# Optimization experiments

Hardware: AMD Instinct MI355X
Metric: run time of the kernel (lower is better)

Reference implementation:

```python
import jax, jax.numpy as jnp
import numpy as np
import math
from functools import partial

SIGMA0 = 12.0
KSIZE = int(2 * (4.0 * SIGMA0 + 0.5))  # 97, already odd
if KSIZE % 2 == 0:
    KSIZE -= 1


def _gauss1d(ksize, sigma):
    # kornia-style gaussian; ksize is odd so no half-pixel shift
    x = jnp.arange(ksize, dtype=jnp.float32) - ksize // 2
    g = jnp.exp(-(x ** 2) / (2.0 * sigma ** 2))
    return g / g.sum()


def _blur(x, sigma):
    # x: (N,1,H,W). filter2d with outer(kx,ky) kernel and constant(zero) border
    # == two separable 1D convs with zero 'SAME' padding.
    k = _gauss1d(KSIZE, sigma)
    dn = ('NCHW', 'OIHW', 'NCHW')
    x = jax.lax.conv_general_dilated(x, k[None, None, :, None], (1, 1), 'SAME', dimension_numbers=dn)
    x = jax.lax.conv_general_dilated(x, k[None, None, None, :], (1, 1), 'SAME', dimension_numbers=dn)
    return x


def _grid_sample_bilinear(img, grid):
    # img: (N,C,H,W); grid: (N,H,W,2) with last dim (x,y) in [-1,1], align_corners=True
    N, C, H, W = img.shape
    x = (grid[..., 0] + 1.0) * 0.5 * (W - 1)
    y = (grid[..., 1] + 1.0) * 0.5 * (H - 1)
    x0 = jnp.floor(x); y0 = jnp.floor(y)
    wx = x - x0; wy = y - y0
    x0i = jnp.clip(x0, 0, W - 1).astype(jnp.int32)
    x1i = jnp.clip(x0 + 1, 0, W - 1).astype(jnp.int32)
    y0i = jnp.clip(y0, 0, H - 1).astype(jnp.int32)
    y1i = jnp.clip(y0 + 1, 0, H - 1).astype(jnp.int32)
    flat = img.reshape(N, C, H * W)

    def gather(yi, xi):
        idx = (yi * W + xi).reshape(N, 1, H * W)
        return jnp.take_along_axis(flat, idx, axis=2).reshape(N, C, H, W)

    wx = wx[:, None]; wy = wy[:, None]  # broadcast over C
    top = gather(y0i, x0i) * (1 - wx) + gather(y0i, x1i) * wx
    bot = gather(y1i, x0i) * (1 - wx) + gather(y1i, x1i) * wx
    return top * (1 - wy) + bot * wy


def _elastic(t, d_rand, sigma, alpha):
    # t: (1,C,H,W); d_rand: (1,2,H,W) uniform [0,1]
    n, c, h, w = t.shape
    d = d_rand * 2.0 - 1.0
    dy = _blur(d[:, 0:1], sigma[0]) * alpha[0]   # (1,1,H,W)
    dx = _blur(d[:, 1:2], sigma[1]) * alpha[1]
    d_yx = jnp.concatenate([dy, dx], axis=1).transpose(0, 2, 3, 1)  # (1,H,W,2) = (dy,dx)
    xs = jnp.linspace(-1.0, 1.0, w, dtype=t.dtype)
    ys = jnp.linspace(-1.0, 1.0, h, dtype=t.dtype)
    gx, gy = jnp.meshgrid(xs, ys)  # (H,W)
    grid = jnp.stack([gx, gy], axis=-1)[None]  # (1,H,W,2) (x,y)
    # NOTE: faithful to source: dy is added to x-coord, dx to y-coord
    return _grid_sample_bilinear(t, jnp.clip(grid + d_yx, -1.0, 1.0))


def setup_inputs() -> dict:
    key = jax.random.key(0)
    k1, k2, k3 = jax.random.split(key, 3)
    H = W = 2048
    return {
        'image': jax.random.normal(k1, (3, H, W), dtype=jnp.float32),
        'mask': (jax.random.uniform(k2, (1, H, W)) > 0.5).astype(jnp.float32),
        'd_rand': jax.random.uniform(k3, (1, 2, H, W), dtype=jnp.float32),
        'log_sigma': jnp.full((2,), math.log(12.0), dtype=jnp.float32),
        'log_alpha': jnp.zeros((2,), dtype=jnp.float32),
    }


def reference(image, mask, d_rand, log_sigma, log_alpha):
    sigma = jnp.exp(log_sigma)
    alpha = jnp.exp(log_alpha)
    img_out = _elastic(image[None], d_rand, sigma, alpha)[0]
    msk_out = _elastic(mask[None], d_rand, sigma, alpha)[0]
    return (img_out, msk_out)
```

## Files before the change

### kernel.cpp

```cpp
#include <hip/hip_runtime.h>

#define H 2048
#define W 2048
#define KS 97
#define KH 48
#define KPAD 112
#define TR 16

__global__ __launch_bounds__(128) void make_weights_k(const float* __restrict__ log_sigma,
                                                      const float* __restrict__ log_alpha,
                                                      float* __restrict__ wts) {
    __shared__ float e0s[KS], e1s[KS];
    __shared__ float sums[2];
    const int t = threadIdx.x;
    const float s0 = expf(log_sigma[0]);
    const float s1 = expf(log_sigma[1]);
    if (t < KS) {
        const float xx = (float)(t - KH);
        e0s[t] = expf(-(xx * xx) / (2.f * s0 * s0));
        e1s[t] = expf(-(xx * xx) / (2.f * s1 * s1));
    }
    __syncthreads();
    if (t == 0) {
        float a = 0.f, b = 0.f;
        for (int k = 0; k < KS; ++k) { a += e0s[k]; b += e1s[k]; }
        sums[0] = a; sums[1] = b;
    }
    __syncthreads();
    if (t < KPAD) {
        wts[t]        = (t < KS) ? e0s[t] / sums[0] : 0.f;
        wts[KPAD + t] = (t < KS) ? e1s[t] / sums[1] : 0.f;
    }
    if (t == 0) {
        wts[2 * KPAD]     = expf(log_alpha[0]);
        wts[2 * KPAD + 1] = expf(log_alpha[1]);
    }
}

__global__ __launch_bounds__(256) void pack_k(const float* __restrict__ image,
                                              const float* __restrict__ mask,
                                              float4* __restrict__ packed) {
    const size_t HW = (size_t)H * W;
    const size_t idx = (size_t)blockIdx.x * 256 + threadIdx.x;
    packed[idx] = make_float4(image[idx], image[HW + idx], image[2 * HW + idx], mask[idx]);
}

template <bool GUARD>
__device__ __forceinline__ float2 vload_row(const float* __restrict__ src, int row, int col) {
    float2 v = make_float2(0.f, 0.f);
    if (!GUARD || ((unsigned)row < (unsigned)H)) {
        const float2 r2 = *(const float2*)(src + (size_t)row * W + col);
        v.x = fmaf(r2.x, 2.f, -1.f);
        v.y = fmaf(r2.y, 2.f, -1.f);
    }
    return v;
}

template <bool GUARD>
__device__ __forceinline__ void vblur_body(const float* __restrict__ src,
                                           const float* __restrict__ g,
                                           float* __restrict__ dst,
                                           int col, int i0) {
    const int base = i0 - KH;
    float2 win[16];
    float2 acc[TR];
#pragma unroll
    for (int t = 0; t < TR; ++t) acc[t] = make_float2(0.f, 0.f);
#pragma unroll
    for (int t = 0; t < 15; ++t) win[t] = vload_row<GUARD>(src, base + t, col);

    for (int m = 0; m < KPAD / 16; ++m) {
        const int kb = m * 16;
#pragma unroll
        for (int r = 0; r < 16; ++r) {
            const int k = kb + r;
            win[(r + 15) & 15] = vload_row<GUARD>(src, base + k + 15, col);
            const float gk = g[k];
#pragma unroll
            for (int t = 0; t < TR; ++t) {
                const float2 u = win[(r + t) & 15];
                acc[t].x = fmaf(gk, u.x, acc[t].x);
                acc[t].y = fmaf(gk, u.y, acc[t].y);
            }
        }
    }
#pragma unroll
    for (int t = 0; t < TR; ++t)
        *(float2*)(dst + (size_t)(i0 + t) * W + col) = acc[t];
}

__global__ __launch_bounds__(256, 4) void vblur_k(const float* __restrict__ drand,
                                                  const float* __restrict__ wts,
                                                  float* __restrict__ tmp) {
    const int c   = blockIdx.z;
    const int col = (blockIdx.x * 256 + threadIdx.x) * 2;
    const int i0  = blockIdx.y * TR;
    const float* __restrict__ src = drand + (size_t)c * H * W;
    const float* __restrict__ g   = wts + c * KPAD;
    float* __restrict__ dst       = tmp + (size_t)c * H * W;

    if (i0 >= KH && i0 + (KPAD - 1 + 15 - KH) <= H - 1)
        vblur_body<false>(src, g, dst, col, i0);
    else
        vblur_body<true>(src, g, dst, col, i0);
}

#define SW 2160
template <bool PACKED>
__global__ __launch_bounds__(512) void hblur_sample_k(const float* __restrict__ tmp,
                                                      const float* __restrict__ wts,
                                                      const float* __restrict__ image,
                                                      const float* __restrict__ mask,
                                                      const float4* __restrict__ packed,
                                                      float* __restrict__ out) {
    const int i   = blockIdx.x;
    const int tid = threadIdx.x;

    __shared__ __align__(16) float s0[SW];
    __shared__ __align__(16) float s1[SW];
    __shared__ __align__(16) float g0s[KPAD];
    __shared__ __align__(16) float g1s[KPAD];

    if (tid < KPAD) { g0s[tid] = wts[tid]; g1s[tid] = wts[KPAD + tid]; }

    const float* __restrict__ t0 = tmp + (size_t)i * W;
    const float* __restrict__ t1 = tmp + (size_t)H * W + (size_t)i * W;
    for (int idx = tid; idx < SW / 4; idx += 512) {
        const int colb = idx * 4 - KH;
        float4 v0 = make_float4(0.f, 0.f, 0.f, 0.f);
        float4 v1 = v0;
        if (colb >= 0 && colb + 3 < W) {
            v0 = *(const float4*)(t0 + colb);
            v1 = *(const float4*)(t1 + colb);
        }
        *(float4*)(s0 + idx * 4) = v0;
        *(float4*)(s1 + idx * 4) = v1;
    }
    __syncthreads();

    const int lb = tid * 4;

    float4 A0 = *(const float4*)(s0 + lb), B0 = *(const float4*)(s0 + lb + 4);
    float4 A1 = *(const float4*)(s1 + lb), B1 = *(const float4*)(s1 + lb + 4);
    float dy[4] = {0.f, 0.f, 0.f, 0.f}, dx[4] = {0.f, 0.f, 0.f, 0.f};

#pragma unroll
    for (int kg = 0; kg < 26; ++kg) {
        const int k0 = kg * 4;
        const float4 g0q = *(const float4*)(g0s + k0);
        const float4 g1q = *(const float4*)(g1s + k0);
        const float4 N0  = *(const float4*)(s0 + lb + k0 + 8);
        const float4 N1  = *(const float4*)(s1 + lb + k0 + 8);
        const float e0[8] = {A0.x, A0.y, A0.z, A0.w, B0.x, B0.y, B0.z, B0.w};
        const float e1[8] = {A1.x, A1.y, A1.z, A1.w, B1.x, B1.y, B1.z, B1.w};
#pragma unroll
        for (int j = 0; j < 4; ++j) {
            const float gj0 = j == 0 ? g0q.x : j == 1 ? g0q.y : j == 2 ? g0q.z : g0q.w;
            const float gj1 = j == 0 ? g1q.x : j == 1 ? g1q.y : j == 2 ? g1q.z : g1q.w;
#pragma unroll
            for (int c = 0; c < 4; ++c) {
                dy[c] = fmaf(gj0, e0[c + j], dy[c]);
                dx[c] = fmaf(gj1, e1[c + j], dx[c]);
            }
        }
        A0 = B0; B0 = N0; A1 = B1; B1 = N1;
    }

    const float a0 = wts[2 * KPAD];
    const float a1 = wts[2 * KPAD + 1];
    const float step = 2.f / 2047.f;
    float res[4][4];
#pragma unroll
    for (int c = 0; c < 4; ++c) {
        const int j = lb + c;
        const float dyc = dy[c] * a0;
        const float dxc = dx[c] * a1;
        float xn = -1.f + (float)j * step + dyc;
        float yn = -1.f + (float)i * step + dxc;
        xn = fminf(fmaxf(xn, -1.f), 1.f);
        yn = fminf(fmaxf(yn, -1.f), 1.f);

        const float x = (xn + 1.f) * 0.5f * (float)(W - 1);
        const float y = (yn + 1.f) * 0.5f * (float)(H - 1);
        const float x0f = floorf(x), y0f = floorf(y);
        const float wx = x - x0f, wy = y - y0f;

        int x0 = (int)x0f, y0 = (int)y0f;
        int x1 = x0 + 1, y1 = y0 + 1;
        x0 = min(max(x0, 0), W - 1); x1 = min(max(x1, 0), W - 1);
        y0 = min(max(y0, 0), H - 1); y1 = min(max(y1, 0), H - 1);

        const float w00 = (1.f - wx) * (1.f - wy);
        const float w10 = wx * (1.f - wy);
        const float w01 = (1.f - wx) * wy;
        const float w11 = wx * wy;

        const size_t i00 = (size_t)y0 * W + x0;
        const size_t i10 = (size_t)y0 * W + x1;
        const size_t i01 = (size_t)y1 * W + x0;
        const size_t i11 = (size_t)y1 * W + x1;

        if (PACKED) {
            const float4 v00 = packed[i00], v10 = packed[i10];
            const float4 v01 = packed[i01], v11 = packed[i11];
            res[0][c] = v00.x * w00 + v10.x * w10 + v01.x * w01 + v11.x * w11;
            res[1][c] = v00.y * w00 + v10.y * w10 + v01.y * w01 + v11.y * w11;
            res[2][c] = v00.z * w00 + v10.z * w10 + v01.z * w01 + v11.z * w11;
            res[3][c] = v00.w * w00 + v10.w * w10 + v01.w * w01 + v11.w * w11;
        } else {
#pragma unroll
            for (int p = 0; p < 3; ++p) {
                const float* __restrict__ pl = image + (size_t)p * H * W;
                res[p][c] = pl[i00] * w00 + pl[i10] * w10 + pl[i01] * w01 + pl[i11] * w11;
            }
            res[3][c] = mask[i00] * w00 + mask[i10] * w10 + mask[i01] * w01 + mask[i11] * w11;
        }
    }

    const size_t o = (size_t)i * W + lb;
#pragma unroll
    for (int p = 0; p < 4; ++p)
        *(float4*)(out + (size_t)p * H * W + o) =
            make_float4(res[p][0], res[p][1], res[p][2], res[p][3]);
}

extern "C" void kernel_launch(void* const* d_in, const int* in_sizes, int n_in,
                              void* d_out, int out_size, void* d_ws, size_t ws_size,
                              hipStream_t stream) {
    const float* image     = (const float*)d_in[0];
    const float* mask      = (const float*)d_in[1];
    const float* drand     = (const float*)d_in[2];
    const float* log_sigma = (const float*)d_in[3];
    const float* log_alpha = (const float*)d_in[4];
    float* out = (float*)d_out;

    const size_t HW = (size_t)H * W;
    const bool can_pack = ws_size >= (6 * HW + 256) * sizeof(float);

    float4* packed; float* tmp; float* wts;
    if (can_pack) {
        packed = (float4*)d_ws;
        tmp    = (float*)d_ws + 4 * HW;
        wts    = tmp + 2 * HW;
    } else {
        packed = nullptr;
        tmp    = (float*)d_ws;
        wts    = tmp + 2 * HW;
    }

    make_weights_k<<<1, 128, 0, stream>>>(log_sigma, log_alpha, wts);
    if (can_pack)
        pack_k<<<(int)(HW / 256), 256, 0, stream>>>(image, mask, packed);
    vblur_k<<<dim3(W / 512, H / TR, 2), 256, 0, stream>>>(drand, wts, tmp);
    if (can_pack)
        hblur_sample_k<true><<<H, 512, 0, stream>>>(tmp, wts, image, mask, packed, out);
    else
        hblur_sample_k<false><<<H, 512, 0, stream>>>(tmp, wts, image, mask, packed, out);
}
```

Measured before the change: 265.9 us.

## Fuse pack and vertical blur into one launch with XCD-aware block remapping

Merges the image/mask packing kernel and the vertical blur kernel into a single launch, with the first blocks doing the blur and the rest doing the packing. Packing now moves four pixels per thread using float4 loads. Block indices are remapped so that contiguous row bands land on the same XCD, for both the blur and the hblur/sample kernel. The aim is to remove one launch, let the two memory-bound phases overlap, and improve L2 locality per XCD. The cost is a mixed-role kernel whose blocks share one launch-bounds/register budget, and a remapping that assumes round-robin dispatch of blocks across the eight XCDs.

```diff
diff --git a/kernel.cpp b/kernel.cpp
--- a/kernel.cpp
+++ b/kernel.cpp
@@ -6,6 +6,8 @@
 #define KH 48
 #define KPAD 112
 #define TR 16
+#define NB_VB 1024
+#define NB_PK 4096
 
 __global__ __launch_bounds__(128) void make_weights_k(const float* __restrict__ log_sigma,
                                                       const float* __restrict__ log_alpha,
@@ -37,14 +39,6 @@
     }
 }
 
-__global__ __launch_bounds__(256) void pack_k(const float* __restrict__ image,
-                                              const float* __restrict__ mask,
-                                              float4* __restrict__ packed) {
-    const size_t HW = (size_t)H * W;
-    const size_t idx = (size_t)blockIdx.x * 256 + threadIdx.x;
-    packed[idx] = make_float4(image[idx], image[HW + idx], image[2 * HW + idx], mask[idx]);
-}
-
 template <bool GUARD>
 __device__ __forceinline__ float2 vload_row(const float* __restrict__ src, int row, int col) {
     float2 v = make_float2(0.f, 0.f);
@@ -89,20 +83,41 @@
         *(float2*)(dst + (size_t)(i0 + t) * W + col) = acc[t];
 }
 
-__global__ __launch_bounds__(256, 4) void vblur_k(const float* __restrict__ drand,
-                                                  const float* __restrict__ wts,
-                                                  float* __restrict__ tmp) {
-    const int c   = blockIdx.z;
-    const int col = (blockIdx.x * 256 + threadIdx.x) * 2;
-    const int i0  = blockIdx.y * TR;
-    const float* __restrict__ src = drand + (size_t)c * H * W;
-    const float* __restrict__ g   = wts + c * KPAD;
-    float* __restrict__ dst       = tmp + (size_t)c * H * W;
-
-    if (i0 >= KH && i0 + (KPAD - 1 + 15 - KH) <= H - 1)
-        vblur_body<false>(src, g, dst, col, i0);
-    else
-        vblur_body<true>(src, g, dst, col, i0);
+__global__ __launch_bounds__(256, 4) void pv_k(const float* __restrict__ drand,
+                                               const float* __restrict__ wts,
+                                               const float* __restrict__ image,
+                                               const float* __restrict__ mask,
+                                               float* __restrict__ tmp,
+                                               float4* __restrict__ packed) {
+    const size_t HW = (size_t)H * W;
+    const int bid = blockIdx.x;
+    if (bid < NB_VB) {
+        const int c   = bid >> 9;
+        const int id  = bid & 511;
+        const int xcd = id & 7;
+        const int seq = id >> 3;
+        const int yb  = xcd * 16 + (seq >> 2);
+        const int xb  = seq & 3;
+        const int col = (xb * 256 + threadIdx.x) * 2;
+        const int i0  = yb * TR;
+        const float* __restrict__ src = drand + (size_t)c * HW;
+        const float* __restrict__ g   = wts + c * KPAD;
+        float* __restrict__ dst       = tmp + (size_t)c * HW;
+        if (i0 >= KH && i0 + 78 <= H - 1)
+            vblur_body<false>(src, g, dst, col, i0);
+        else
+            vblur_body<true>(src, g, dst, col, i0);
+    } else {
+        const size_t idx4 = ((size_t)(bid - NB_VB) * 256 + threadIdx.x) * 4;
+        const float4 p0 = *(const float4*)(image + idx4);
+        const float4 p1 = *(const float4*)(image + HW + idx4);
+        const float4 p2 = *(const float4*)(image + 2 * HW + idx4);
+        const float4 pm = *(const float4*)(mask + idx4);
+        packed[idx4 + 0] = make_float4(p0.x, p1.x, p2.x, pm.x);
+        packed[idx4 + 1] = make_float4(p0.y, p1.y, p2.y, pm.y);
+        packed[idx4 + 2] = make_float4(p0.z, p1.z, p2.z, pm.z);
+        packed[idx4 + 3] = make_float4(p0.w, p1.w, p2.w, pm.w);
+    }
 }
 
 #define SW 2160
@@ -113,7 +128,7 @@
                                                       const float* __restrict__ mask,
                                                       const float4* __restrict__ packed,
                                                       float* __restrict__ out) {
-    const int i   = blockIdx.x;
+    const int i   = (blockIdx.x & 7) * 256 + (blockIdx.x >> 3);
     const int tid = threadIdx.x;
 
     __shared__ __align__(16) float s0[SW];
@@ -249,9 +264,8 @@
     }
 
     make_weights_k<<<1, 128, 0, stream>>>(log_sigma, log_alpha, wts);
-    if (can_pack)
-        pack_k<<<(int)(HW / 256), 256, 0, stream>>>(image, mask, packed);
-    vblur_k<<<dim3(W / 512, H / TR, 2), 256, 0, stream>>>(drand, wts, tmp);
+    pv_k<<<can_pack ? (NB_VB + NB_PK) : NB_VB, 256, 0, stream>>>(drand, wts, image, mask,
+                                                                 tmp, packed);
     if (can_pack)
         hblur_sample_k<true><<<H, 512, 0, stream>>>(tmp, wts, image, mask, packed, out);
     else
```

Result: faster. 246.1 us (-7.5%).
